# Kernel optimization log

Measured on AMD Instinct MI355X. Metric: run time of the kernel, lower is better.

Reference implementation:

```python
import jax, jax.numpy as jnp
import numpy as np

N_HEAD = 16
N_KV_HEAD = 4
HEAD_DIM = 64  # n_embd // n_head = 1024 // 16
N_EMBD = 1024


def _alibi_bias(T, n_head, head_dim):
    # slopes: start = 2**(-2**(-(log2(H)-3))); slope_i = start**(i+1)
    start = 2.0 ** (-2.0 ** (-(np.log2(n_head) - 3.0)))
    slopes = jnp.asarray(start ** np.arange(1, n_head + 1), dtype=jnp.float32)  # [H]
    rel = (jnp.arange(T, dtype=jnp.float32)[None, :]
           - jnp.arange(T, dtype=jnp.float32)[:, None])  # [T,T], rel[i,j] = j - i
    bias = slopes[:, None, None] * rel[None, :, :]  # [H,T,T]
    # Faithful to the torch module: masked_fill(-inf) is then OVERWRITTEN by
    # torch.tril, which zeroes the upper triangle. Net effect: lower-tri alibi
    # values, 0 above the diagonal (NO causal masking).
    bias = jnp.tril(bias)
    return bias * (head_dim ** -0.5)  # extra scale applied in forward


def setup_inputs() -> dict:
    key = jax.random.key(0)
    ks = jax.random.split(key, 5)
    B, T, C = 4, 2048, N_EMBD
    w_scale = 0.02
    return {
        "x": jax.random.normal(ks[0], (B, T, C), dtype=jnp.float32),
        "Wq": jax.random.normal(ks[1], (C, C), dtype=jnp.float32) * w_scale,
        "Wkv": jax.random.normal(ks[2], (2 * N_KV_HEAD * HEAD_DIM, C), dtype=jnp.float32) * w_scale,
        "Wproj": jax.random.normal(ks[3], (C, C), dtype=jnp.float32) * w_scale,
        "bproj": jnp.zeros((C,), dtype=jnp.float32),
    }


def reference(x, Wq, Wkv, Wproj, bproj):
    B, T, C = x.shape
    H, KVH, D = N_HEAD, N_KV_HEAD, HEAD_DIM
    ratio = H // KVH

    q = jnp.einsum('btc,ec->bte', x, Wq).reshape(B, T, H, D).transpose(0, 2, 1, 3)  # [B,H,T,D]
    kv = jnp.einsum('btc,ec->bte', x, Wkv)  # [B,T,2*KVH*D]
    k, v = jnp.split(kv, 2, axis=-1)
    k = k.reshape(B, T, KVH, D).transpose(0, 2, 1, 3)  # [B,KVH,T,D]
    v = v.reshape(B, T, KVH, D).transpose(0, 2, 1, 3)
    # torch .repeat tiles whole blocks: query head h uses kv head h % KVH
    k = jnp.tile(k, (1, ratio, 1, 1))  # [B,H,T,D]
    v = jnp.tile(v, (1, ratio, 1, 1))

    bias = _alibi_bias(T, H, D)  # [H,T,T], already *= D**-0.5
    scores = jnp.einsum('bhtd,bhsd->bhts', q, k) * (D ** -0.5) + bias[None]
    attn = jax.nn.softmax(scores, axis=-1)
    out = jnp.einsum('bhts,bhsd->bhtd', attn, v)  # [B,H,T,D]
    out = out.transpose(0, 2, 1, 3).reshape(B, T, C)
    return jnp.einsum('btc,ec->bte', out, Wproj) + bproj
```

## Files before the change

kernel.cpp:

```cpp
#include <hip/hip_runtime.h>
#include <hip/hip_bf16.h>
#include <cstdint>

typedef __bf16 bf16;
typedef bf16 bf16x2 __attribute__((ext_vector_type(2)));
typedef bf16 bf16x4 __attribute__((ext_vector_type(4)));
typedef bf16 bf16x8 __attribute__((ext_vector_type(8)));
typedef float f32x4 __attribute__((ext_vector_type(4)));
typedef unsigned int uint32x2_t __attribute__((ext_vector_type(2)));
typedef unsigned int uint32x4_t __attribute__((ext_vector_type(4)));

#define MFMA16(a, b, c) __builtin_amdgcn_mfma_f32_16x16x32_bf16((a), (b), (c), 0, 0, 0)

#define QSCALE 0.18033688011112042f

__device__ inline void async16(const bf16* g, bf16* l) {
  __builtin_amdgcn_global_load_lds(
      (const __attribute__((address_space(1))) void*)g,
      (__attribute__((address_space(3))) void*)l, 16, 0, 0);
}

__global__ void cast_all(const float* __restrict__ x, const float* __restrict__ wq,
                         const float* __restrict__ wkv, const float* __restrict__ wp,
                         bf16* __restrict__ xb, bf16* __restrict__ w1b,
                         bf16* __restrict__ wpb) {
  const int i = blockIdx.x * blockDim.x + threadIdx.x;
  const float4* src;
  bf16x4* dst;
  int idx;
  if (i < 2097152) {
    src = (const float4*)x; dst = (bf16x4*)xb; idx = i;
  } else if (i < 2359296) {
    src = (const float4*)wq; dst = (bf16x4*)w1b; idx = i - 2097152;
  } else if (i < 2490368) {
    src = (const float4*)wkv; dst = (bf16x4*)(w1b + 1048576); idx = i - 2359296;
  } else {
    src = (const float4*)wp; dst = (bf16x4*)wpb; idx = i - 2490368;
  }
  const float4 v = src[idx];
  bf16x4 o;
  o.x = (bf16)v.x; o.y = (bf16)v.y; o.z = (bf16)v.z; o.w = (bf16)v.w;
  dst[idx] = o;
}

__global__ __launch_bounds__(256, 2)
void gemm_qkv(const bf16* __restrict__ A, const bf16* __restrict__ B,
              bf16* __restrict__ qb, bf16* __restrict__ kb, bf16* __restrict__ vb) {
  constexpr int K = 1024;
  constexpr int NX = 12;
  __shared__ bf16 sA[128 * 64];
  __shared__ bf16 sB[128 * 64];
  const int tid = threadIdx.x;
  const int lane = tid & 63, wid = tid >> 6;
  const int col = lane & 15, quad = lane >> 4;
  const int wm = wid >> 1, wn = wid & 1;
  const int bid = blockIdx.y * NX + blockIdx.x;
  const int swz = (bid & 7) * (NX * 64 / 8) + (bid >> 3);
  const int m0 = (swz / NX) * 128, n0 = (swz % NX) * 128;
  const int c7 = col & 7;

  f32x4 acc[4][4];
  const f32x4 z = {0.f, 0.f, 0.f, 0.f};
#pragma unroll
  for (int mi = 0; mi < 4; mi++)
#pragma unroll
    for (int ni = 0; ni < 4; ni++) acc[mi][ni] = z;

  for (int k0 = 0; k0 < K; k0 += 64) {
    __syncthreads();
#pragma unroll
    for (int c = 0; c < 4; ++c) {
      const int idx = c * 256 + tid;
      const int row = idx >> 3, kc = idx & 7;
      const int gkc = kc ^ (row & 7);
      async16(&A[(size_t)(m0 + row) * K + k0 + gkc * 8], &sA[idx * 8]);
      async16(&B[(size_t)(n0 + row) * K + k0 + gkc * 8], &sB[idx * 8]);
    }
    __syncthreads();
#pragma unroll
    for (int ks = 0; ks < 2; ++ks) {
      bf16x8 af[4], bfr[4];
#pragma unroll
      for (int i = 0; i < 4; i++)
        af[i] = *(const bf16x8*)&sA[(wm * 64 + i * 16 + col) * 64 +
                                    (((ks * 4 + quad) ^ c7) << 3)];
#pragma unroll
      for (int i = 0; i < 4; i++)
        bfr[i] = *(const bf16x8*)&sB[(wn * 64 + i * 16 + col) * 64 +
                                     (((ks * 4 + quad) ^ c7) << 3)];
#pragma unroll
      for (int mi = 0; mi < 4; mi++)
#pragma unroll
        for (int ni = 0; ni < 4; ni++)
          acc[mi][ni] = MFMA16(af[mi], bfr[ni], acc[mi][ni]);
    }
  }
#pragma unroll
  for (int mi = 0; mi < 4; mi++) {
#pragma unroll
    for (int ni = 0; ni < 4; ni++) {
      const int e = n0 + wn * 64 + ni * 16 + col;
#pragma unroll
      for (int r = 0; r < 4; r++) {
        const int m = m0 + wm * 64 + mi * 16 + quad * 4 + r;
        const int bb = m >> 11, t = m & 2047;
        if (e < 1024) {
          qb[(((size_t)bb * 16 + (e >> 6)) * 2048 + t) * 64 + (e & 63)] =
              (bf16)(acc[mi][ni][r] * QSCALE);
        } else if (e < 1280) {
          const int f = e - 1024;
          kb[(((size_t)bb * 4 + (f >> 6)) * 2048 + t) * 64 + (f & 63)] =
              (bf16)acc[mi][ni][r];
        } else {
          const int f = e - 1280;
          vb[(((size_t)bb * 4 + (f >> 6)) * 2048 + t) * 64 + (f & 63)] =
              (bf16)acc[mi][ni][r];
        }
      }
    }
  }
}

__global__ __launch_bounds__(256, 2)
void gemm_proj(const bf16* __restrict__ A, const bf16* __restrict__ B,
               const float* __restrict__ bias, float* __restrict__ out) {
  constexpr int K = 1024;
  constexpr int NX = 8;
  __shared__ bf16 sA[128 * 64];
  __shared__ bf16 sB[128 * 64];
  const int tid = threadIdx.x;
  const int lane = tid & 63, wid = tid >> 6;
  const int col = lane & 15, quad = lane >> 4;
  const int wm = wid >> 1, wn = wid & 1;
  const int bid = blockIdx.y * NX + blockIdx.x;
  const int swz = (bid & 7) * (NX * 64 / 8) + (bid >> 3);
  const int m0 = (swz / NX) * 128, n0 = (swz % NX) * 128;
  const int c7 = col & 7;

  f32x4 acc[4][4];
  const f32x4 z = {0.f, 0.f, 0.f, 0.f};
#pragma unroll
  for (int mi = 0; mi < 4; mi++)
#pragma unroll
    for (int ni = 0; ni < 4; ni++) acc[mi][ni] = z;

  for (int k0 = 0; k0 < K; k0 += 64) {
    __syncthreads();
#pragma unroll
    for (int c = 0; c < 4; ++c) {
      const int idx = c * 256 + tid;
      const int row = idx >> 3, kc = idx & 7;
      const int gkc = kc ^ (row & 7);
      async16(&A[(size_t)(m0 + row) * K + k0 + gkc * 8], &sA[idx * 8]);
      async16(&B[(size_t)(n0 + row) * K + k0 + gkc * 8], &sB[idx * 8]);
    }
    __syncthreads();
#pragma unroll
    for (int ks = 0; ks < 2; ++ks) {
      bf16x8 af[4], bfr[4];
#pragma unroll
      for (int i = 0; i < 4; i++)
        af[i] = *(const bf16x8*)&sA[(wm * 64 + i * 16 + col) * 64 +
                                    (((ks * 4 + quad) ^ c7) << 3)];
#pragma unroll
      for (int i = 0; i < 4; i++)
        bfr[i] = *(const bf16x8*)&sB[(wn * 64 + i * 16 + col) * 64 +
                                     (((ks * 4 + quad) ^ c7) << 3)];
#pragma unroll
      for (int mi = 0; mi < 4; mi++)
#pragma unroll
        for (int ni = 0; ni < 4; ni++)
          acc[mi][ni] = MFMA16(af[mi], bfr[ni], acc[mi][ni]);
    }
  }
#pragma unroll
  for (int mi = 0; mi < 4; mi++) {
#pragma unroll
    for (int ni = 0; ni < 4; ni++) {
      const int e = n0 + wn * 64 + ni * 16 + col;
      const float be = bias[e];
#pragma unroll
      for (int r = 0; r < 4; r++) {
        const int m = m0 + wm * 64 + mi * 16 + quad * 4 + r;
        out[(size_t)m * 1024 + e] = acc[mi][ni][r] + be;
      }
    }
  }
}

#define SM_HALF(kp_)                                                        \
  _Pragma("unroll")                                                         \
  for (int ni = 0; ni < 4; ni++) {                                          \
    unsigned plo[2], phi[2];                                                \
    _Pragma("unroll")                                                       \
    for (int t = 0; t < 2; t++) {                                           \
      const int mi = (kp_) * 2 + t;                                         \
      const int U = c0s + mi * 16 - qbase - ni * 16;                        \
      f32x4 p;                                                              \
      if (U <= -15) {                                                       \
        const float bb = cb * (float)(U + qoff);                            \
        _Pragma("unroll")                                                   \
        for (int r = 0; r < 4; r++)                                         \
          p[r] = __builtin_amdgcn_exp2f(S[mi][ni][r] + (bb + cb * (float)r)); \
      } else if (U >= 16) {                                                 \
        _Pragma("unroll")                                                   \
        for (int r = 0; r < 4; r++)                                         \
          p[r] = __builtin_amdgcn_exp2f(S[mi][ni][r]);                      \
      } else {                                                              \
        const float relf = (float)(U + qoff);                               \
        _Pragma("unroll")                                                   \
        for (int r = 0; r < 4; r++) {                                       \
          const float rr = relf + (float)r;                                 \
          const float bb = (rr <= 0.f) ? cb * rr : 0.f;                     \
          p[r] = __builtin_amdgcn_exp2f(S[mi][ni][r] + bb);                 \
        }                                                                   \
      }                                                                     \
      bf16x2 lo, hi;                                                        \
      lo.x = (bf16)p[0]; lo.y = (bf16)p[1];                                 \
      hi.x = (bf16)p[2]; hi.y = (bf16)p[3];                                 \
      plo[t] = __builtin_bit_cast(unsigned, lo);                            \
      phi[t] = __builtin_bit_cast(unsigned, hi);                            \
    }                                                                       \
    uint32x2_t rl = __builtin_amdgcn_permlane32_swap(plo[0], plo[1], false, false); \
    uint32x2_t rh = __builtin_amdgcn_permlane32_swap(phi[0], phi[1], false, false); \
    uint32x2_t w02 = __builtin_amdgcn_permlane16_swap(rl.x, rl.y, false, false);    \
    uint32x2_t w13 = __builtin_amdgcn_permlane16_swap(rh.x, rh.y, false, false);    \
    uint32x4_t W;                                                           \
    W.x = w02.x; W.y = w13.x; W.z = w02.y; W.w = w13.y;                     \
    ap[ni][kp_] = __builtin_bit_cast(bf16x8, W);                            \
  }

#define PV_HALF(kp_)                                                        \
  {                                                                         \
    bf16x8 bv[4];                                                           \
    _Pragma("unroll")                                                       \
    for (int nd = 0; nd < 4; nd++) {                                        \
      const int d = nd * 16 + col;                                          \
      bv[nd] = *(const bf16x8*)&svw[d * 136 + rbase +                       \
                   ((((kp_) * 4 + quad) ^ (d >> 3)) << 3)];                 \
    }                                                                       \
    __builtin_amdgcn_s_setprio(1);                                          \
    _Pragma("unroll")                                                       \
    for (int mi = 0; mi < 4; mi++) {                                        \
      _Pragma("unroll")                                                     \
      for (int nd = 0; nd < 4; nd++)                                        \
        O[mi][nd] = MFMA16(ap[mi][kp_], bv[nd], O[mi][nd]);                 \
      Osum[mi] = MFMA16(ap[mi][kp_], bones, Osum[mi]);                      \
    }                                                                       \
    __builtin_amdgcn_s_setprio(0);                                          \
  }

__global__ __launch_bounds__(256, 2)
void attn_alibi(const bf16* __restrict__ qb, const bf16* __restrict__ kb,
                const bf16* __restrict__ vb, bf16* __restrict__ ob) {
  __shared__ bf16 sK[2][128 * 64];
  __shared__ bf16 sVt[2][64 * 136];
  const int tid = threadIdx.x;
  const int lane = tid & 63, wid = tid >> 6;
  const int col = lane & 15, quad = lane >> 4;
  const int c7 = col & 7;
  const int bh = blockIdx.y;
  const int b = bh >> 4, h = bh & 15, kvh = h & 3;
  const int qbase = __builtin_amdgcn_readfirstlane(blockIdx.x * 256 + wid * 64);

  const bf16* qptr = qb + ((size_t)(b * 16 + h) * 2048 + qbase) * 64;
  const bf16* kptr = kb + ((size_t)(b * 4 + kvh) * 2048) * 64;
  const bf16* vptr = vb + ((size_t)(b * 4 + kvh) * 2048) * 64;

  bf16x8 bq[4][2];
#pragma unroll
  for (int ni = 0; ni < 4; ni++)
#pragma unroll
    for (int ks = 0; ks < 2; ks++)
      bq[ni][ks] = *(const bf16x8*)&qptr[(ni * 16 + col) * 64 + ks * 32 + quad * 8];

  bf16x8 bones;
#pragma unroll
  for (int j = 0; j < 8; j++) bones[j] = (bf16)1.0f;

  f32x4 O[4][4];
  f32x4 Osum[4];
  const f32x4 z = {0.f, 0.f, 0.f, 0.f};
#pragma unroll
  for (int mi = 0; mi < 4; mi++) {
    Osum[mi] = z;
#pragma unroll
    for (int nd = 0; nd < 4; nd++) O[mi][nd] = z;
  }

  const float cb = exp2f(-0.5f * (float)(h + 1)) * QSCALE;
  const int qoff = quad * 4 - col;

  const int rowA = tid >> 3, kc = tid & 7;
  const int kxA = (kc ^ (rowA & 7)) << 3;
  const int rv = rowA * 2;
  const int blkv = rv >> 3, rlv = rv & 7;

  async16(&kptr[(size_t)(rowA) * 64 + kxA], &sK[0][tid * 8]);
  async16(&kptr[(size_t)(rowA + 32) * 64 + kxA], &sK[0][(256 + tid) * 8]);
  async16(&kptr[(size_t)(rowA + 64) * 64 + kxA], &sK[0][(512 + tid) * 8]);
  async16(&kptr[(size_t)(rowA + 96) * 64 + kxA], &sK[0][(768 + tid) * 8]);
  bf16x8 vrA0 = *(const bf16x8*)&vptr[(size_t)rv * 64 + kc * 8];
  bf16x8 vrA1 = *(const bf16x8*)&vptr[(size_t)(rv + 1) * 64 + kc * 8];
  bf16x8 vrB0 = *(const bf16x8*)&vptr[(size_t)(64 + rv) * 64 + kc * 8];
  bf16x8 vrB1 = *(const bf16x8*)&vptr[(size_t)(64 + rv + 1) * 64 + kc * 8];

  int bufi = 0;
  for (int c0 = 0; c0 < 2048; c0 += 128, bufi ^= 1) {
    bf16* skw = sK[bufi];
    bf16* svw = sVt[bufi];
#pragma unroll
    for (int j = 0; j < 8; j++) {
      bf16x2 pa;
      pa.x = vrA0[j];
      pa.y = vrA1[j];
      *(bf16x2*)&svw[(kc * 8 + j) * 136 + ((blkv ^ kc) << 3) + rlv] = pa;
      bf16x2 pb;
      pb.x = vrB0[j];
      pb.y = vrB1[j];
      *(bf16x2*)&svw[(kc * 8 + j) * 136 + 64 + ((blkv ^ kc) << 3) + rlv] = pb;
    }
    __syncthreads();

    {
      const int cn = (c0 + 128 < 2048) ? c0 + 128 : 0;
      bf16* skn = sK[bufi ^ 1];
      async16(&kptr[(size_t)(cn + rowA) * 64 + kxA], &skn[tid * 8]);
      async16(&kptr[(size_t)(cn + rowA + 32) * 64 + kxA], &skn[(256 + tid) * 8]);
      async16(&kptr[(size_t)(cn + rowA + 64) * 64 + kxA], &skn[(512 + tid) * 8]);
      async16(&kptr[(size_t)(cn + rowA + 96) * 64 + kxA], &skn[(768 + tid) * 8]);
      vrA0 = *(const bf16x8*)&vptr[(size_t)(cn + rv) * 64 + kc * 8];
      vrA1 = *(const bf16x8*)&vptr[(size_t)(cn + rv + 1) * 64 + kc * 8];
      vrB0 = *(const bf16x8*)&vptr[(size_t)(cn + 64 + rv) * 64 + kc * 8];
      vrB1 = *(const bf16x8*)&vptr[(size_t)(cn + 64 + rv + 1) * 64 + kc * 8];
    }

#pragma unroll
    for (int sub = 0; sub < 2; sub++) {
      const int rbase = sub * 64;
      const int c0s = c0 + rbase;

      f32x4 S[4][4];
      {
        bf16x8 ak[4];
#pragma unroll
        for (int mi = 0; mi < 4; mi++)
          ak[mi] = *(const bf16x8*)&skw[(rbase + mi * 16 + col) * 64 +
                                        ((quad ^ c7) << 3)];
        __builtin_amdgcn_s_setprio(1);
#pragma unroll
        for (int mi = 0; mi < 4; mi++)
#pragma unroll
          for (int ni = 0; ni < 4; ni++)
            S[mi][ni] = MFMA16(ak[mi], bq[ni][0], z);
        __builtin_amdgcn_s_setprio(0);
#pragma unroll
        for (int mi = 0; mi < 4; mi++)
          ak[mi] = *(const bf16x8*)&skw[(rbase + mi * 16 + col) * 64 +
                                        (((4 + quad) ^ c7) << 3)];
        __builtin_amdgcn_s_setprio(1);
#pragma unroll
        for (int mi = 0; mi < 4; mi++)
#pragma unroll
          for (int ni = 0; ni < 4; ni++)
            S[mi][ni] = MFMA16(ak[mi], bq[ni][1], S[mi][ni]);
        __builtin_amdgcn_s_setprio(0);
      }

      bf16x8 ap[4][2];
      SM_HALF(0);
      PV_HALF(0);
      SM_HALF(1);
      PV_HALF(1);
    }
  }

#pragma unroll
  for (int mi = 0; mi < 4; mi++) {
#pragma unroll
    for (int r = 0; r < 4; r++) {
      const float inv = 1.0f / Osum[mi][r];
      const int t = qbase + mi * 16 + quad * 4 + r;
#pragma unroll
      for (int nd = 0; nd < 4; nd++) {
        ob[((size_t)b * 2048 + t) * 1024 + h * 64 + nd * 16 + col] =
            (bf16)(O[mi][nd][r] * inv);
      }
    }
  }
}

extern "C" void kernel_launch(void* const* d_in, const int* in_sizes, int n_in,
                              void* d_out, int out_size, void* d_ws, size_t ws_size,
                              hipStream_t stream) {
  const float* x     = (const float*)d_in[0];
  const float* Wq    = (const float*)d_in[1];
  const float* Wkv   = (const float*)d_in[2];
  const float* Wproj = (const float*)d_in[3];
  const float* bproj = (const float*)d_in[4];
  float* out = (float*)d_out;

  bf16* xb  = (bf16*)d_ws;
  bf16* w1b = xb  + 8388608;
  bf16* wpb = w1b + 1572864;
  bf16* qb  = wpb + 1048576;
  bf16* kb  = qb  + 8388608;
  bf16* vb  = kb  + 2097152;
  bf16* aob = vb  + 2097152;

  cast_all<<<10752, 256, 0, stream>>>(x, Wq, Wkv, Wproj, xb, w1b, wpb);
  gemm_qkv<<<dim3(12, 64), 256, 0, stream>>>(xb, w1b, qb, kb, vb);
  attn_alibi<<<dim3(8, 64), 256, 0, stream>>>(qb, kb, vb, aob);
  gemm_proj<<<dim3(8, 64), 256, 0, stream>>>(aob, wpb, bproj, out);
}
```

Baseline: 258.9 us.

## Shrink attention KV tile from 128 to 64 keys and drop setprio hints

Each loop iteration of the attention kernel now stages 64 keys instead of 128, halving the K and transposed-V shared-memory buffers and removing the inner two-way sub-tile loop. The s_setprio calls around the MFMA blocks are also removed. The intent is to cut LDS footprint and register pressure, possibly improving occupancy or scheduling. In exchange it doubles the number of __syncthreads barriers and prefetch rounds per key sweep, and the MFMA blocks lose their raised wave priority.

```diff
diff --git a/kernel.cpp b/kernel.cpp
--- a/kernel.cpp
+++ b/kernel.cpp
@@ -195,7 +195,7 @@
     _Pragma("unroll")                                                       \
     for (int t = 0; t < 2; t++) {                                           \
       const int mi = (kp_) * 2 + t;                                         \
-      const int U = c0s + mi * 16 - qbase - ni * 16;                        \
+      const int U = c0 + mi * 16 - qbase - ni * 16;                         \
       f32x4 p;                                                              \
       if (U <= -15) {                                                       \
         const float bb = cb * (float)(U + qoff);                            \
@@ -236,10 +236,9 @@
     _Pragma("unroll")                                                       \
     for (int nd = 0; nd < 4; nd++) {                                        \
       const int d = nd * 16 + col;                                          \
-      bv[nd] = *(const bf16x8*)&svw[d * 136 + rbase +                       \
+      bv[nd] = *(const bf16x8*)&svw[d * 72 +                                \
                    ((((kp_) * 4 + quad) ^ (d >> 3)) << 3)];                 \
     }                                                                       \
-    __builtin_amdgcn_s_setprio(1);                                          \
     _Pragma("unroll")                                                       \
     for (int mi = 0; mi < 4; mi++) {                                        \
       _Pragma("unroll")                                                     \
@@ -247,14 +246,13 @@
         O[mi][nd] = MFMA16(ap[mi][kp_], bv[nd], O[mi][nd]);                 \
       Osum[mi] = MFMA16(ap[mi][kp_], bones, Osum[mi]);                      \
     }                                                                       \
-    __builtin_amdgcn_s_setprio(0);                                          \
   }
 
 __global__ __launch_bounds__(256, 2)
 void attn_alibi(const bf16* __restrict__ qb, const bf16* __restrict__ kb,
                 const bf16* __restrict__ vb, bf16* __restrict__ ob) {
-  __shared__ bf16 sK[2][128 * 64];
-  __shared__ bf16 sVt[2][64 * 136];
+  __shared__ bf16 sK[2][64 * 64];
+  __shared__ bf16 sVt[2][64 * 72];
   const int tid = threadIdx.x;
   const int lane = tid & 63, wid = tid >> 6;
   const int col = lane & 15, quad = lane >> 4;
@@ -296,83 +294,59 @@
   const int rv = rowA * 2;
   const int blkv = rv >> 3, rlv = rv & 7;
 
-  async16(&kptr[(size_t)(rowA) * 64 + kxA], &sK[0][tid * 8]);
+  async16(&kptr[(size_t)rowA * 64 + kxA], &sK[0][tid * 8]);
   async16(&kptr[(size_t)(rowA + 32) * 64 + kxA], &sK[0][(256 + tid) * 8]);
-  async16(&kptr[(size_t)(rowA + 64) * 64 + kxA], &sK[0][(512 + tid) * 8]);
-  async16(&kptr[(size_t)(rowA + 96) * 64 + kxA], &sK[0][(768 + tid) * 8]);
-  bf16x8 vrA0 = *(const bf16x8*)&vptr[(size_t)rv * 64 + kc * 8];
-  bf16x8 vrA1 = *(const bf16x8*)&vptr[(size_t)(rv + 1) * 64 + kc * 8];
-  bf16x8 vrB0 = *(const bf16x8*)&vptr[(size_t)(64 + rv) * 64 + kc * 8];
-  bf16x8 vrB1 = *(const bf16x8*)&vptr[(size_t)(64 + rv + 1) * 64 + kc * 8];
+  bf16x8 vr0 = *(const bf16x8*)&vptr[(size_t)rv * 64 + kc * 8];
+  bf16x8 vr1 = *(const bf16x8*)&vptr[(size_t)(rv + 1) * 64 + kc * 8];
 
   int bufi = 0;
-  for (int c0 = 0; c0 < 2048; c0 += 128, bufi ^= 1) {
+  for (int c0 = 0; c0 < 2048; c0 += 64, bufi ^= 1) {
     bf16* skw = sK[bufi];
     bf16* svw = sVt[bufi];
 #pragma unroll
     for (int j = 0; j < 8; j++) {
-      bf16x2 pa;
-      pa.x = vrA0[j];
-      pa.y = vrA1[j];
-      *(bf16x2*)&svw[(kc * 8 + j) * 136 + ((blkv ^ kc) << 3) + rlv] = pa;
-      bf16x2 pb;
-      pb.x = vrB0[j];
-      pb.y = vrB1[j];
-      *(bf16x2*)&svw[(kc * 8 + j) * 136 + 64 + ((blkv ^ kc) << 3) + rlv] = pb;
+      bf16x2 pr;
+      pr.x = vr0[j];
+      pr.y = vr1[j];
+      *(bf16x2*)&svw[(kc * 8 + j) * 72 + ((blkv ^ kc) << 3) + rlv] = pr;
     }
     __syncthreads();
 
     {
-      const int cn = (c0 + 128 < 2048) ? c0 + 128 : 0;
+      const int cn = (c0 + 64 < 2048) ? c0 + 64 : 0;
       bf16* skn = sK[bufi ^ 1];
       async16(&kptr[(size_t)(cn + rowA) * 64 + kxA], &skn[tid * 8]);
       async16(&kptr[(size_t)(cn + rowA + 32) * 64 + kxA], &skn[(256 + tid) * 8]);
-      async16(&kptr[(size_t)(cn + rowA + 64) * 64 + kxA], &skn[(512 + tid) * 8]);
-      async16(&kptr[(size_t)(cn + rowA + 96) * 64 + kxA], &skn[(768 + tid) * 8]);
-      vrA0 = *(const bf16x8*)&vptr[(size_t)(cn + rv) * 64 + kc * 8];
-      vrA1 = *(const bf16x8*)&vptr[(size_t)(cn + rv + 1) * 64 + kc * 8];
-      vrB0 = *(const bf16x8*)&vptr[(size_t)(cn + 64 + rv) * 64 + kc * 8];
-      vrB1 = *(const bf16x8*)&vptr[(size_t)(cn + 64 + rv + 1) * 64 + kc * 8];
-    }
-
-#pragma unroll
-    for (int sub = 0; sub < 2; sub++) {
-      const int rbase = sub * 64;
-      const int c0s = c0 + rbase;
-
-      f32x4 S[4][4];
-      {
-        bf16x8 ak[4];
-#pragma unroll
-        for (int mi = 0; mi < 4; mi++)
-          ak[mi] = *(const bf16x8*)&skw[(rbase + mi * 16 + col) * 64 +
-                                        ((quad ^ c7) << 3)];
-        __builtin_amdgcn_s_setprio(1);
-#pragma unroll
-        for (int mi = 0; mi < 4; mi++)
-#pragma unroll
-          for (int ni = 0; ni < 4; ni++)
-            S[mi][ni] = MFMA16(ak[mi], bq[ni][0], z);
-        __builtin_amdgcn_s_setprio(0);
-#pragma unroll
-        for (int mi = 0; mi < 4; mi++)
-          ak[mi] = *(const bf16x8*)&skw[(rbase + mi * 16 + col) * 64 +
-                                        (((4 + quad) ^ c7) << 3)];
-        __builtin_amdgcn_s_setprio(1);
-#pragma unroll
-        for (int mi = 0; mi < 4; mi++)
-#pragma unroll
-          for (int ni = 0; ni < 4; ni++)
-            S[mi][ni] = MFMA16(ak[mi], bq[ni][1], S[mi][ni]);
-        __builtin_amdgcn_s_setprio(0);
-      }
-
-      bf16x8 ap[4][2];
-      SM_HALF(0);
-      PV_HALF(0);
-      SM_HALF(1);
-      PV_HALF(1);
-    }
+      vr0 = *(const bf16x8*)&vptr[(size_t)(cn + rv) * 64 + kc * 8];
+      vr1 = *(const bf16x8*)&vptr[(size_t)(cn + rv + 1) * 64 + kc * 8];
+    }
+
+    f32x4 S[4][4];
+    {
+      bf16x8 ak[4];
+#pragma unroll
+      for (int mi = 0; mi < 4; mi++)
+        ak[mi] = *(const bf16x8*)&skw[(mi * 16 + col) * 64 + ((quad ^ c7) << 3)];
+#pragma unroll
+      for (int mi = 0; mi < 4; mi++)
+#pragma unroll
+        for (int ni = 0; ni < 4; ni++)
+          S[mi][ni] = MFMA16(ak[mi], bq[ni][0], z);
+#pragma unroll
+      for (int mi = 0; mi < 4; mi++)
+        ak[mi] = *(const bf16x8*)&skw[(mi * 16 + col) * 64 + (((4 + quad) ^ c7) << 3)];
+#pragma unroll
+      for (int mi = 0; mi < 4; mi++)
+#pragma unroll
+        for (int ni = 0; ni < 4; ni++)
+          S[mi][ni] = MFMA16(ak[mi], bq[ni][1], S[mi][ni]);
+    }
+
+    bf16x8 ap[4][2];
+    SM_HALF(0);
+    PV_HALF(0);
+    SM_HALF(1);
+    PV_HALF(1);
   }
 
 #pragma unroll
```

New measurement: 240.8 us. 1.08x faster.
